# Kernel tuning notes

Hardware: AMD Instinct MI355X
Metric: run time of the kernel (lower is better)

Reference implementation:

```python
import jax, jax.numpy as jnp
import numpy as np

B, C, H, W = 64, 2048, 14, 14
D, S, ITERS, EPS, HID = 256, 8, 3, 1e-8, 512


def build_pos(h, w, d):
    gy, gx = np.meshgrid(np.arange(h), np.arange(w), indexing='ij')
    q = d // 4
    omega = 1.0 / (10000.0 ** (np.arange(q) / q))
    ey = gy.reshape(-1, 1) * omega
    ex = gx.reshape(-1, 1) * omega
    pe = np.concatenate([np.sin(ey), np.cos(ey), np.sin(ex), np.cos(ex)], axis=1)
    return jnp.asarray(pe[None], jnp.float32)  # (1, h*w, d)


def layernorm(x, g, b, eps=1e-5):
    m = x.mean(-1, keepdims=True)
    v = ((x - m) ** 2).mean(-1, keepdims=True)
    return (x - m) * jax.lax.rsqrt(v + eps) * g + b


def setup_inputs() -> dict:
    key = jax.random.key(0)
    ks = jax.random.split(key, 16)
    w = lambda k, shp, s=0.02: jax.random.normal(k, shp, jnp.float32) * s
    inp = {
        'x': jax.random.normal(ks[0], (B, C, H, W), jnp.float32),
        'slot_noise': jax.random.normal(ks[1], (B, S, D), jnp.float32),
        'conv_w': w(ks[2], (C, D)), 'conv_b': jnp.zeros((D,), jnp.float32),
        'pos': build_pos(H, W, D),
        'slots_mu': jax.random.normal(ks[3], (1, 1, D), jnp.float32),
        'slots_logsigma': -jnp.ones((1, 1, D), jnp.float32),
        'qw': w(ks[4], (D, D)), 'qb': jnp.zeros((D,), jnp.float32),
        'kw': w(ks[5], (D, D)), 'kb': jnp.zeros((D,), jnp.float32),
        'vw': w(ks[6], (D, D)), 'vb': jnp.zeros((D,), jnp.float32),
        'gru_wih': w(ks[7], (D, 3 * D)), 'gru_whh': w(ks[8], (D, 3 * D)),
        'gru_bih': jnp.zeros((3 * D,), jnp.float32), 'gru_bhh': jnp.zeros((3 * D,), jnp.float32),
        'w1': w(ks[9], (D, HID)), 'b1': jnp.zeros((HID,), jnp.float32),
        'w2': w(ks[10], (HID, D)), 'b2': jnp.zeros((D,), jnp.float32),
        'ln_in_g': jnp.ones((D,), jnp.float32), 'ln_in_b': jnp.zeros((D,), jnp.float32),
        'ln_s_g': jnp.ones((D,), jnp.float32), 'ln_s_b': jnp.zeros((D,), jnp.float32),
        'ln_ff_g': jnp.ones((D,), jnp.float32), 'ln_ff_b': jnp.zeros((D,), jnp.float32),
    }
    return inp


def reference(x, slot_noise, conv_w, conv_b, pos, slots_mu, slots_logsigma,
              qw, qb, kw, kb, vw, vb, gru_wih, gru_whh, gru_bih, gru_bhh,
              w1, b1, w2, b2, ln_in_g, ln_in_b, ln_s_g, ln_s_b, ln_ff_g, ln_ff_b):
    b, c, h, w_ = x.shape
    d = qw.shape[0]
    scale = d ** (-0.5)
    # (B,C,H,W) -> (B,N,C) -> project -> add pos
    xt = x.transpose(0, 2, 3, 1).reshape(b, h * w_, c)
    xt = xt @ conv_w + conv_b + pos
    # slot init
    slots = slots_mu + jnp.exp(slots_logsigma) * slot_noise  # (B,S,D)
    inp = layernorm(xt, ln_in_g, ln_in_b)
    k = inp @ kw + kb
    v = inp @ vw + vb
    attn = None
    for _ in range(ITERS):
        slots_prev = slots
        s = layernorm(slots, ln_s_g, ln_s_b)
        q = s @ qw + qb
        dots = jnp.einsum('bid,bjd->bij', q, k) * scale  # (B,S,N)
        attn = jax.nn.softmax(dots, axis=1) + EPS  # softmax over slots
        attn = attn / attn.sum(-1, keepdims=True)  # renormalize over keys
        updates = jnp.einsum('bjd,bij->bid', v, attn)  # (B,S,D)
        # GRUCell (torch semantics)
        gi = updates @ gru_wih + gru_bih
        gh = slots_prev @ gru_whh + gru_bhh
        ir, iz, inn = jnp.split(gi, 3, axis=-1)
        hr, hz, hn = jnp.split(gh, 3, axis=-1)
        r = jax.nn.sigmoid(ir + hr)
        z = jax.nn.sigmoid(iz + hz)
        nn_ = jnp.tanh(inn + r * hn)
        slots = (1.0 - z) * nn_ + z * slots_prev
        ff = layernorm(slots, ln_ff_g, ln_ff_b)
        slots = slots + (jax.nn.relu(ff @ w1 + b1)) @ w2 + b2
    attn_map = attn.reshape(b, S, h, w_)
    return slots, attn_map
```

## Files before the change

### kernel.cpp

```cpp
#include <hip/hip_runtime.h>
#include <stdint.h>

#define HWN 196
#define CIN 2048
#define DD  256
#define BB  64
#define NSLOT 8
#define KVPAD 224
#define MTOT 12544
#define BKP 128

typedef __attribute__((ext_vector_type(8))) short short8;
typedef __attribute__((ext_vector_type(4))) float f32x4;
typedef __attribute__((ext_vector_type(4))) unsigned short us4;

__device__ __forceinline__ ushort f2bf(float f){ union{float f;uint32_t u;}v;v.f=f;uint32_t u=v.u;return (ushort)((u+0x7FFFu+((u>>16)&1u))>>16);}
__device__ __forceinline__ float bf2f(ushort h){ union{uint32_t u;float f;}v;v.u=((uint32_t)h)<<16;return v.f;}
__device__ __forceinline__ float sigm(float x){ return 1.f/(1.f+expf(-x)); }

__device__ __forceinline__ short8 ldsY(const ushort* buf, int LD, int kt, int lane){
    int row = lane & 15;
    int ch = kt*4 + (lane>>4);
    return *(const short8*)&buf[row*LD + ((ch ^ (row&7))<<3)];
}
__device__ __forceinline__ short8 gX(const ushort* base, int K, int nrow, int kt, int lane){
    return *(const short8*)&base[(size_t)nrow*K + kt*32 + (lane>>4)*8];
}

struct TD { const float* s; ushort* d; int R, C, t0; };
struct TD8 { TD a[8]; };

__global__ __launch_bounds__(256) void k_prep(TD8 td){
    __shared__ float tile[32][33];
    int bt = blockIdx.x;
    int mi = 0;
    #pragma unroll
    for (int i = 1; i < 8; ++i) if (bt >= td.a[i].t0) mi = i;
    TD d = td.a[mi];
    int lt = bt - d.t0;
    int tilesx = (d.C + 31) >> 5;
    int cb = (lt % tilesx) * 32, rb = (lt / tilesx) * 32;
    int tx = threadIdx.x & 31, ty = threadIdx.x >> 5;
    for (int i = ty; i < 32; i += 8) {
        int r = rb + i, c = cb + tx;
        tile[i][tx] = (r < d.R && c < d.C) ? d.s[(size_t)r * d.C + c] : 0.f;
    }
    __syncthreads();
    for (int i = ty; i < 32; i += 8) {
        int c = cb + i, r = rb + tx;
        if (c < d.C && r < d.R) d.d[(size_t)c * d.R + r] = f2bf(tile[tx][i]);
    }
}

__global__ __launch_bounds__(512) void k_proj(const float* __restrict__ x,
        const ushort* __restrict__ cwT, float* __restrict__ Cpart){
    __shared__ ushort As[2][64*BKP];
    const int t = threadIdx.x, lane = t & 63, wv = t >> 6;
    const int tile = blockIdx.x >> 1, kq = blockIdx.x & 1;
    const int bm = tile * 64;
    const int kbase = kq * 1024;

    const int am = t & 63, kg = t >> 6;
    const int mg = bm + am;
    const int ab = mg / HWN, ap = mg % HWN;
    const float* aptr = x + (size_t)ab*(CIN*HWN) + ap + (size_t)kbase*HWN;

    f32x4 acc[4][2] = {};
    float areg[16];

    #pragma unroll
    for (int j = 0; j < 16; ++j) areg[j] = aptr[(size_t)(kg*16+j)*HWN];
    {
        short8 av0, av1;
        #pragma unroll
        for (int j = 0; j < 8; ++j){ av0[j] = (short)f2bf(areg[j]); av1[j] = (short)f2bf(areg[8+j]); }
        int ch0 = kg*2;
        *(short8*)&As[0][am*BKP + ((ch0^(am&7))<<3)] = av0;
        *(short8*)&As[0][am*BKP + (((ch0+1)^(am&7))<<3)] = av1;
    }
    __syncthreads();
    int cur = 0;
    for (int kt = 0; kt < 8; ++kt){
        if (kt < 7){
            #pragma unroll
            for (int j = 0; j < 16; ++j)
                areg[j] = aptr[(size_t)((kt+1)*BKP + kg*16+j)*HWN];
        }
        short8 bfr[4][2];
        #pragma unroll
        for (int kk = 0; kk < 4; ++kk)
            #pragma unroll
            for (int ni = 0; ni < 2; ++ni){
                int n = wv*32 + ni*16 + (lane&15);
                bfr[kk][ni] = *(const short8*)&cwT[(size_t)n*CIN + kbase + kt*BKP + kk*32 + (lane>>4)*8];
            }
        #pragma unroll
        for (int kk = 0; kk < 4; ++kk){
            short8 afr[4];
            #pragma unroll
            for (int mi = 0; mi < 4; ++mi){
                int row = mi*16 + (lane&15);
                int ch = kk*4 + (lane>>4);
                afr[mi] = *(const short8*)&As[cur][row*BKP + ((ch^(row&7))<<3)];
            }
            #pragma unroll
            for (int mi = 0; mi < 4; ++mi)
                #pragma unroll
                for (int ni = 0; ni < 2; ++ni)
                    acc[mi][ni] = __builtin_amdgcn_mfma_f32_16x16x32_bf16(afr[mi], bfr[kk][ni], acc[mi][ni], 0,0,0);
        }
        if (kt < 7){
            short8 av0, av1;
            #pragma unroll
            for (int j = 0; j < 8; ++j){ av0[j] = (short)f2bf(areg[j]); av1[j] = (short)f2bf(areg[8+j]); }
            int ch0 = kg*2;
            *(short8*)&As[cur^1][am*BKP + ((ch0^(am&7))<<3)] = av0;
            *(short8*)&As[cur^1][am*BKP + (((ch0+1)^(am&7))<<3)] = av1;
        }
        __syncthreads();
        cur ^= 1;
    }
    float* outp = Cpart + (size_t)kq*MTOT*DD;
    #pragma unroll
    for (int mi = 0; mi < 4; ++mi){
        #pragma unroll
        for (int ni = 0; ni < 2; ++ni){
            int n = wv*32 + ni*16 + (lane&15);
            #pragma unroll
            for (int r = 0; r < 4; ++r){
                int m = bm + mi*16 + (lane>>4)*4 + r;
                outp[(size_t)m*DD + n] = acc[mi][ni][r];
            }
        }
    }
}

__global__ __launch_bounds__(512) void k_red(const float* __restrict__ Cpart,
        const float* __restrict__ cb, const float* __restrict__ pos,
        const float* __restrict__ lng, const float* __restrict__ lnb,
        const ushort* __restrict__ kwT, const ushort* __restrict__ vwT,
        const float* __restrict__ kb, const float* __restrict__ vb,
        ushort* __restrict__ kbf, ushort* __restrict__ vT){
    __shared__ ushort As[32*256];
    const int t = threadIdx.x, lane = t & 63, wv = t >> 6;
    const int b = blockIdx.x / 7, pblk = blockIdx.x % 7;
    {
        int row = t >> 4, seg = t & 15;
        int pin = pblk*32 + row;
        int grow = b*HWN + pin;
        if (grow > MTOT-1) grow = MTOT-1;
        int p = pin < HWN ? pin : HWN-1;
        const float* c0 = Cpart + (size_t)grow*DD + seg*16;
        const float* c1 = Cpart + (size_t)MTOT*DD + (size_t)grow*DD + seg*16;
        const float* pp = pos + (size_t)p*DD + seg*16;
        float f[16];
        float s = 0.f, sq = 0.f;
        #pragma unroll
        for (int q = 0; q < 4; ++q){
            f32x4 a  = *(const f32x4*)&c0[q*4];
            f32x4 bq = *(const f32x4*)&c1[q*4];
            f32x4 pv = *(const f32x4*)&pp[q*4];
            f32x4 cv = *(const f32x4*)&cb[seg*16 + q*4];
            #pragma unroll
            for (int r2 = 0; r2 < 4; ++r2){
                float v = a[r2] + bq[r2] + pv[r2] + cv[r2];
                f[q*4+r2] = v; s += v; sq += v*v;
            }
        }
        #pragma unroll
        for (int m = 8; m >= 1; m >>= 1){ s += __shfl_xor(s, m, 64); sq += __shfl_xor(sq, m, 64); }
        float mean = s * (1.f/256.f);
        float rs = rsqrtf(sq*(1.f/256.f) - mean*mean + 1e-5f);
        int d0 = seg*16;
        short8 o0, o1;
        #pragma unroll
        for (int j = 0; j < 8; ++j){
            o0[j] = (short)f2bf((f[j]   - mean)*rs*lng[d0+j]   + lnb[d0+j]);
            o1[j] = (short)f2bf((f[8+j] - mean)*rs*lng[d0+8+j] + lnb[d0+8+j]);
        }
        int ch0 = seg*2;
        *(short8*)&As[row*256 + ((ch0^(row&7))<<3)] = o0;
        *(short8*)&As[row*256 + (((ch0+1)^(row&7))<<3)] = o1;
    }
    __syncthreads();
    f32x4 acck[2][2] = {}, accv[2][2] = {};
    const int n0 = wv*32;
    #pragma unroll
    for (int kt = 0; kt < 8; ++kt){
        short8 afr[2];
        #pragma unroll
        for (int mi = 0; mi < 2; ++mi){
            int row = mi*16 + (lane&15);
            int ch = kt*4 + (lane>>4);
            afr[mi] = *(const short8*)&As[row*256 + ((ch^(row&7))<<3)];
        }
        #pragma unroll
        for (int ni = 0; ni < 2; ++ni){
            int n = n0 + ni*16 + (lane&15);
            int koff = kt*32 + (lane>>4)*8;
            short8 bk = *(const short8*)&kwT[(size_t)n*DD + koff];
            short8 bv = *(const short8*)&vwT[(size_t)n*DD + koff];
            #pragma unroll
            for (int mi = 0; mi < 2; ++mi){
                acck[mi][ni] = __builtin_amdgcn_mfma_f32_16x16x32_bf16(afr[mi], bk, acck[mi][ni],0,0,0);
                accv[mi][ni] = __builtin_amdgcn_mfma_f32_16x16x32_bf16(afr[mi], bv, accv[mi][ni],0,0,0);
            }
        }
    }
    #pragma unroll
    for (int mi = 0; mi < 2; ++mi){
        #pragma unroll
        for (int ni = 0; ni < 2; ++ni){
            int n = n0 + ni*16 + (lane&15);
            float kbn = kb[n], vbn = vb[n];
            int pl0 = pblk*32 + mi*16 + (lane>>4)*4;
            us4 pk;
            #pragma unroll
            for (int r = 0; r < 4; ++r){
                kbf[((size_t)b*KVPAD + pl0 + r)*DD + n] = f2bf(acck[mi][ni][r] + kbn);
                pk[r] = f2bf(accv[mi][ni][r] + vbn);
            }
            *(us4*)&vT[((size_t)b*DD + n)*KVPAD + pl0] = pk;
        }
    }
}

__global__ __launch_bounds__(512) void k_init(const float* __restrict__ noise,
        const float* __restrict__ mu, const float* __restrict__ lsig,
        const ushort* __restrict__ qwT, const float* __restrict__ qb,
        const float* __restrict__ gs, const float* __restrict__ bs,
        float* __restrict__ slots, ushort* __restrict__ qbuf){
    __shared__ float Sld[16*256];
    __shared__ ushort Ysn[16*256];
    __shared__ float part[8][16][2];
    __shared__ float stats[16][2];
    const int t = threadIdx.x, lane = t & 63, w = t >> 6;
    const int bb = blockIdx.x, rbase = bb*16;
    {
        int row = t>>5, ch = t&31; int d = ch*8;
        f32x4 n0 = *(const f32x4*)&noise[(size_t)(rbase+row)*DD + d];
        f32x4 n1 = *(const f32x4*)&noise[(size_t)(rbase+row)*DD + d + 4];
        f32x4 m0 = *(const f32x4*)&mu[d];
        f32x4 m1 = *(const f32x4*)&mu[d+4];
        f32x4 l0 = *(const f32x4*)&lsig[d];
        f32x4 l1 = *(const f32x4*)&lsig[d+4];
        f32x4 s0, s1;
        #pragma unroll
        for (int j = 0; j < 4; ++j){
            s0[j] = m0[j] + expf(l0[j])*n0[j];
            s1[j] = m1[j] + expf(l1[j])*n1[j];
        }
        *(f32x4*)&slots[(size_t)(rbase+row)*DD + d] = s0;
        *(f32x4*)&slots[(size_t)(rbase+row)*DD + d + 4] = s1;
        *(f32x4*)&Sld[row*256 + d] = s0;
        *(f32x4*)&Sld[row*256 + d + 4] = s1;
    }
    __syncthreads();
    f32x4 sv[2];
    #pragma unroll
    for (int sub = 0; sub < 2; ++sub){
        int d0 = w*32 + sub*16 + (lane>>4)*4;
        sv[sub] = *(const f32x4*)&Sld[(lane&15)*256 + d0];
    }
    {
        float lsum = 0.f, lsq = 0.f;
        #pragma unroll
        for (int sub = 0; sub < 2; ++sub)
            #pragma unroll
            for (int r = 0; r < 4; ++r){ float v = sv[sub][r]; lsum += v; lsq += v*v; }
        lsum += __shfl_xor(lsum, 16, 64); lsum += __shfl_xor(lsum, 32, 64);
        lsq  += __shfl_xor(lsq, 16, 64);  lsq  += __shfl_xor(lsq, 32, 64);
        if (lane < 16){ part[w][lane][0] = lsum; part[w][lane][1] = lsq; }
    }
    __syncthreads();
    if (t < 16){
        float a = 0.f, c = 0.f;
        #pragma unroll
        for (int i = 0; i < 8; ++i){ a += part[i][t][0]; c += part[i][t][1]; }
        float mean = a*(1.f/256.f);
        stats[t][0] = mean;
        stats[t][1] = rsqrtf(c*(1.f/256.f) - mean*mean + 1e-5f);
    }
    __syncthreads();
    {
        int slot = lane&15;
        float mean = stats[slot][0], rs = stats[slot][1];
        #pragma unroll
        for (int sub = 0; sub < 2; ++sub){
            int d0 = w*32 + sub*16 + (lane>>4)*4;
            f32x4 g4 = *(const f32x4*)&gs[d0];
            f32x4 b4 = *(const f32x4*)&bs[d0];
            us4 o;
            #pragma unroll
            for (int r = 0; r < 4; ++r) o[r] = f2bf((sv[sub][r]-mean)*rs*g4[r] + b4[r]);
            int ch = d0>>3;
            *(us4*)&Ysn[slot*256 + ((ch^(slot&7))<<3) + (d0&7)] = o;
        }
    }
    __syncthreads();
    f32x4 qa[2] = {};
    #pragma unroll
    for (int kt = 0; kt < 8; ++kt){
        short8 ysn = ldsY(Ysn, 256, kt, lane);
        #pragma unroll
        for (int sub = 0; sub < 2; ++sub){
            int nrow = w*32 + sub*16 + (lane&15);
            short8 xx = gX(qwT, 256, nrow, kt, lane);
            qa[sub] = __builtin_amdgcn_mfma_f32_16x16x32_bf16(xx, ysn, qa[sub], 0,0,0);
        }
    }
    #pragma unroll
    for (int sub = 0; sub < 2; ++sub){
        int qd0 = w*32 + sub*16 + (lane>>4)*4;
        f32x4 qb4 = *(const f32x4*)&qb[qd0];
        us4 o;
        #pragma unroll
        for (int r = 0; r < 4; ++r) o[r] = f2bf((qa[sub][r]+qb4[r])*0.0625f);
        *(us4*)&qbuf[(size_t)(rbase+(lane&15))*DD + qd0] = o;
    }
}

__device__ __forceinline__ float sm_ep(f32x4 acc, int f, int lane, ushort* Xat, int srow){
    int k0 = f*16 + (lane>>4)*4;
    us4 o;
    float ps = 0.f;
    #pragma unroll
    for (int r = 0; r < 4; ++r){
        float v = acc[r];
        float mx = v;
        mx = fmaxf(mx, __shfl_xor(mx, 1, 64));
        mx = fmaxf(mx, __shfl_xor(mx, 2, 64));
        mx = fmaxf(mx, __shfl_xor(mx, 4, 64));
        float e = expf(v - mx);
        float se = e;
        se += __shfl_xor(se, 1, 64);
        se += __shfl_xor(se, 2, 64);
        se += __shfl_xor(se, 4, 64);
        float val = e/se + 1e-8f;
        if (k0 + r >= HWN) val = 0.f;
        ps += val;
        o[r] = f2bf(val);
    }
    int ch = k0 >> 3;
    *(us4*)&Xat[srow*256 + ((ch^(srow&7))<<3) + (k0&7)] = o;
    return ps;
}

__global__ __launch_bounds__(512, 2) void k_slot(
        const ushort* __restrict__ qbuf, const ushort* __restrict__ kbf,
        const ushort* __restrict__ vT, float* __restrict__ slots,
        ushort* __restrict__ qout,
        const ushort* __restrict__ wihT, const ushort* __restrict__ whhT,
        const float* __restrict__ bih, const float* __restrict__ bhh,
        const ushort* __restrict__ w1T, const float* __restrict__ b1,
        const ushort* __restrict__ w2T, const float* __restrict__ b2,
        const float* __restrict__ gff, const float* __restrict__ bff,
        const float* __restrict__ gs, const float* __restrict__ bs,
        const ushort* __restrict__ qwT, const float* __restrict__ qb,
        float* __restrict__ out_slots, float* __restrict__ out_attn,
        int final_){
    __shared__ ushort Yq[16*256];
    __shared__ ushort Xat[16*256];
    __shared__ ushort Yupd[16*256];
    __shared__ ushort Yslb[16*256];
    __shared__ ushort Ysn[16*256];
    __shared__ ushort Yh[16*512];
    __shared__ float wpart[8][16];
    __shared__ float invk[16];
    __shared__ float part[8][16][2];
    __shared__ float stats[16][2];
    const int t = threadIdx.x, lane = t & 63, w = t >> 6;
    const int b = blockIdx.x;
    const int rbase = b * NSLOT;
    const int srow = lane & 15;
    const int srd = (srow < NSLOT) ? srow : 0;

    if (t < 256){
        int row = t>>5, ch = t&31;
        short8 v = *(const short8*)&qbuf[(size_t)(rbase+row)*DD + ch*8];
        *(short8*)&Yq[row*256 + ((ch^(row&7))<<3)] = v;
        f32x4 s0 = *(const f32x4*)&slots[(size_t)(rbase+row)*DD + ch*8];
        f32x4 s1 = *(const f32x4*)&slots[(size_t)(rbase+row)*DD + ch*8 + 4];
        short8 sv;
        #pragma unroll
        for (int j = 0; j < 4; ++j){ sv[j] = (short)f2bf(s0[j]); sv[4+j] = (short)f2bf(s1[j]); }
        *(short8*)&Yslb[row*256 + ((ch^(row&7))<<3)] = sv;
    } else {
        int i = t - 256;
        int row = (i>>5) + 8, ch = i&31;
        short8 z;
        #pragma unroll
        for (int j = 0; j < 8; ++j) z[j] = 0;
        *(short8*)&Yq[row*256 + ((ch^(row&7))<<3)] = z;
        *(short8*)&Yupd[row*256 + ((ch^(row&7))<<3)] = z;
        *(short8*)&Yslb[row*256 + ((ch^(row&7))<<3)] = z;
    }
    __syncthreads();
    {
        short8 yf[8];
        #pragma unroll
        for (int kt = 0; kt < 8; ++kt) yf[kt] = ldsY(Yq, 256, kt, lane);
        const ushort* kb_ = kbf + (size_t)b*KVPAD*DD;
        const int f0 = w, f1 = w + 8;
        const bool v1 = (f1 < 14);
        const int r0 = f0*16 + (lane&15), r1 = f1*16 + (lane&15);
        short8 xa[2], xb[2];
        xa[0] = gX(kb_, 256, r0, 0, lane);
        if (v1) xb[0] = gX(kb_, 256, r1, 0, lane);
        f32x4 accA = {}, accB = {};
        #pragma unroll
        for (int kt = 0; kt < 8; ++kt){
            int cu = kt & 1, nx = cu ^ 1;
            if (kt < 7){
                xa[nx] = gX(kb_, 256, r0, kt+1, lane);
                if (v1) xb[nx] = gX(kb_, 256, r1, kt+1, lane);
            }
            accA = __builtin_amdgcn_mfma_f32_16x16x32_bf16(xa[cu], yf[kt], accA, 0,0,0);
            if (v1) accB = __builtin_amdgcn_mfma_f32_16x16x32_bf16(xb[cu], yf[kt], accB, 0,0,0);
        }
        float ps = sm_ep(accA, f0, lane, Xat, srow);
        if (v1) ps += sm_ep(accB, f1, lane, Xat, srow);
        ps += __shfl_xor(ps, 16, 64);
        ps += __shfl_xor(ps, 32, 64);
        if (lane < 16) wpart[w][lane] = ps;
    }
    __syncthreads();
    if (t < 16){
        float s = 0.f;
        #pragma unroll
        for (int i = 0; i < 8; ++i) s += wpart[i][t];
        invk[t] = 1.f/s;
    }
    f32x4 pvacc[2];
    {
        short8 xat[7];
        #pragma unroll
        for (int kt = 0; kt < 7; ++kt) xat[kt] = ldsY(Xat, 256, kt, lane);
        const ushort* vb_ = vT + (size_t)b*DD*KVPAD;
        const int d0a = (w*2)*16 + (lane&15), d0b = (w*2+1)*16 + (lane&15);
        short8 ya[2], yb[2];
        ya[0] = gX(vb_, KVPAD, d0a, 0, lane);
        yb[0] = gX(vb_, KVPAD, d0b, 0, lane);
        f32x4 aA = {}, aB = {};
        #pragma unroll
        for (int kt = 0; kt < 7; ++kt){
            int cu = kt & 1, nx = cu ^ 1;
            if (kt < 6){
                ya[nx] = gX(vb_, KVPAD, d0a, kt+1, lane);
                yb[nx] = gX(vb_, KVPAD, d0b, kt+1, lane);
            }
            aA = __builtin_amdgcn_mfma_f32_16x16x32_bf16(xat[kt], ya[cu], aA, 0,0,0);
            aB = __builtin_amdgcn_mfma_f32_16x16x32_bf16(xat[kt], yb[cu], aB, 0,0,0);
        }
        pvacc[0] = aA; pvacc[1] = aB;
    }
    __syncthreads();
    {
        f32x4 iv = *(const f32x4*)&invk[(lane>>4)*4];
        #pragma unroll
        for (int i = 0; i < 2; ++i){
            int d0 = (w*2 + i)*16;
            #pragma unroll
            for (int r = 0; r < 4; ++r){
                int s2 = (lane>>4)*4 + r;
                if (s2 < NSLOT){
                    int d = d0 + (lane&15);
                    int ch = d >> 3;
                    Yupd[s2*256 + ((ch^(s2&7))<<3) + (d&7)] = f2bf(pvacc[i][r]*iv[r]);
                }
            }
        }
    }
    if (final_){
        for (int idx = t; idx < NSLOT*HWN; idx += 512){
            int slot = idx/HWN, key = idx - slot*HWN;
            int ch = key >> 3;
            out_attn[(size_t)b*NSLOT*HWN + idx] =
                bf2f(Xat[slot*256 + ((ch^(slot&7))<<3) + (key&7)]) * invk[slot];
        }
    }
    __syncthreads();
    f32x4 gi[6] = {}, gh[6] = {};
    {
        int nrw[6];
        #pragma unroll
        for (int g = 0; g < 3; ++g)
            #pragma unroll
            for (int sub = 0; sub < 2; ++sub)
                nrw[g*2+sub] = g*256 + w*32 + sub*16 + (lane&15);
        short8 xw[2][12];
        #pragma unroll
        for (int j = 0; j < 6; ++j){
            xw[0][j]   = gX(wihT, 256, nrw[j], 0, lane);
            xw[0][6+j] = gX(whhT, 256, nrw[j], 0, lane);
        }
        #pragma unroll
        for (int kt = 0; kt < 8; ++kt){
            int cu = kt & 1, nx = cu ^ 1;
            if (kt < 7){
                #pragma unroll
                for (int j = 0; j < 6; ++j){
                    xw[nx][j]   = gX(wihT, 256, nrw[j], kt+1, lane);
                    xw[nx][6+j] = gX(whhT, 256, nrw[j], kt+1, lane);
                }
            }
            short8 yu = ldsY(Yupd, 256, kt, lane);
            short8 ys = ldsY(Yslb, 256, kt, lane);
            #pragma unroll
            for (int j = 0; j < 6; ++j){
                gi[j] = __builtin_amdgcn_mfma_f32_16x16x32_bf16(xw[cu][j],   yu, gi[j], 0,0,0);
                gh[j] = __builtin_amdgcn_mfma_f32_16x16x32_bf16(xw[cu][6+j], ys, gh[j], 0,0,0);
            }
        }
    }
    f32x4 snew[2];
    #pragma unroll
    for (int sub = 0; sub < 2; ++sub){
        int d0 = w*32 + sub*16 + (lane>>4)*4;
        f32x4 sp  = *(const f32x4*)&slots[(size_t)(rbase + srd)*DD + d0];
        f32x4 bir = *(const f32x4*)&bih[d0];
        f32x4 biz = *(const f32x4*)&bih[256 + d0];
        f32x4 bin = *(const f32x4*)&bih[512 + d0];
        f32x4 bhr = *(const f32x4*)&bhh[d0];
        f32x4 bhz = *(const f32x4*)&bhh[256 + d0];
        f32x4 bhn = *(const f32x4*)&bhh[512 + d0];
        #pragma unroll
        for (int r = 0; r < 4; ++r){
            float ir = gi[0+sub][r] + bir[r];
            float iz = gi[2+sub][r] + biz[r];
            float in_ = gi[4+sub][r] + bin[r];
            float hr = gh[0+sub][r] + bhr[r];
            float hz = gh[2+sub][r] + bhz[r];
            float hn = gh[4+sub][r] + bhn[r];
            float rr = sigm(ir + hr);
            float zz = sigm(iz + hz);
            float nn = tanhf(in_ + rr*hn);
            snew[sub][r] = (1.f - zz)*nn + zz*sp[r];
        }
    }
    {
        float lsum = 0.f, lsq = 0.f;
        #pragma unroll
        for (int sub = 0; sub < 2; ++sub)
            #pragma unroll
            for (int r = 0; r < 4; ++r){ float v = snew[sub][r]; lsum += v; lsq += v*v; }
        lsum += __shfl_xor(lsum, 16, 64); lsum += __shfl_xor(lsum, 32, 64);
        lsq  += __shfl_xor(lsq, 16, 64);  lsq  += __shfl_xor(lsq, 32, 64);
        if (lane < 16){ part[w][lane][0] = lsum; part[w][lane][1] = lsq; }
    }
    __syncthreads();
    if (t < 16){
        float a = 0.f, c = 0.f;
        #pragma unroll
        for (int i = 0; i < 8; ++i){ a += part[i][t][0]; c += part[i][t][1]; }
        float mean = a*(1.f/256.f);
        stats[t][0] = mean;
        stats[t][1] = rsqrtf(c*(1.f/256.f) - mean*mean + 1e-5f);
    }
    __syncthreads();
    {
        float mean = stats[srow][0], rs = stats[srow][1];
        #pragma unroll
        for (int sub = 0; sub < 2; ++sub){
            int d0 = w*32 + sub*16 + (lane>>4)*4;
            f32x4 g4 = *(const f32x4*)&gff[d0];
            f32x4 b4 = *(const f32x4*)&bff[d0];
            us4 o;
            #pragma unroll
            for (int r = 0; r < 4; ++r) o[r] = f2bf((snew[sub][r]-mean)*rs*g4[r] + b4[r]);
            int ch = d0 >> 3;
            *(us4*)&Ysn[srow*256 + ((ch^(srow&7))<<3) + (d0&7)] = o;
        }
    }
    __syncthreads();
    {
        int nr1[4];
        #pragma unroll
        for (int s2 = 0; s2 < 4; ++s2) nr1[s2] = w*64 + s2*16 + (lane&15);
        short8 xw1[2][4];
        #pragma unroll
        for (int s2 = 0; s2 < 4; ++s2) xw1[0][s2] = gX(w1T, 256, nr1[s2], 0, lane);
        f32x4 hh[4] = {};
        #pragma unroll
        for (int kt = 0; kt < 8; ++kt){
            int cu = kt & 1, nx = cu ^ 1;
            if (kt < 7){
                #pragma unroll
                for (int s2 = 0; s2 < 4; ++s2) xw1[nx][s2] = gX(w1T, 256, nr1[s2], kt+1, lane);
            }
            short8 ysn = ldsY(Ysn, 256, kt, lane);
            #pragma unroll
            for (int s2 = 0; s2 < 4; ++s2)
                hh[s2] = __builtin_amdgcn_mfma_f32_16x16x32_bf16(xw1[cu][s2], ysn, hh[s2], 0,0,0);
        }
        #pragma unroll
        for (int s2 = 0; s2 < 4; ++s2){
            int n0 = w*64 + s2*16 + (lane>>4)*4;
            f32x4 b14 = *(const f32x4*)&b1[n0];
            us4 o;
            #pragma unroll
            for (int r = 0; r < 4; ++r) o[r] = f2bf(fmaxf(hh[s2][r] + b14[r], 0.f));
            int ch = n0 >> 3;
            *(us4*)&Yh[srow*512 + ((ch^(srow&7))<<3) + (n0&7)] = o;
        }
    }
    __syncthreads();
    f32x4 ns[2];
    {
        int nr2[2];
        #pragma unroll
        for (int sub = 0; sub < 2; ++sub) nr2[sub] = w*32 + sub*16 + (lane&15);
        short8 xw2[2][2];
        #pragma unroll
        for (int sub = 0; sub < 2; ++sub) xw2[0][sub] = gX(w2T, 512, nr2[sub], 0, lane);
        f32x4 o2[2] = {};
        #pragma unroll
        for (int kt = 0; kt < 16; ++kt){
            int cu = kt & 1, nx = cu ^ 1;
            if (kt < 15){
                #pragma unroll
                for (int sub = 0; sub < 2; ++sub) xw2[nx][sub] = gX(w2T, 512, nr2[sub], kt+1, lane);
            }
            short8 yh = ldsY(Yh, 512, kt, lane);
            #pragma unroll
            for (int sub = 0; sub < 2; ++sub)
                o2[sub] = __builtin_amdgcn_mfma_f32_16x16x32_bf16(xw2[cu][sub], yh, o2[sub], 0,0,0);
        }
        float* dst = final_ ? out_slots : slots;
        #pragma unroll
        for (int sub = 0; sub < 2; ++sub){
            int d0 = w*32 + sub*16 + (lane>>4)*4;
            f32x4 b24 = *(const f32x4*)&b2[d0];
            #pragma unroll
            for (int r = 0; r < 4; ++r) ns[sub][r] = o2[sub][r] + b24[r] + snew[sub][r];
            if (srow < NSLOT)
                *(f32x4*)&dst[(size_t)(rbase + srow)*DD + d0] = ns[sub];
        }
    }
    if (final_) return;
    {
        float lsum = 0.f, lsq = 0.f;
        #pragma unroll
        for (int sub = 0; sub < 2; ++sub)
            #pragma unroll
            for (int r = 0; r < 4; ++r){ float v = ns[sub][r]; lsum += v; lsq += v*v; }
        lsum += __shfl_xor(lsum, 16, 64); lsum += __shfl_xor(lsum, 32, 64);
        lsq  += __shfl_xor(lsq, 16, 64);  lsq  += __shfl_xor(lsq, 32, 64);
        if (lane < 16){ part[w][lane][0] = lsum; part[w][lane][1] = lsq; }
    }
    __syncthreads();
    if (t < 16){
        float a = 0.f, c = 0.f;
        #pragma unroll
        for (int i = 0; i < 8; ++i){ a += part[i][t][0]; c += part[i][t][1]; }
        float mean = a*(1.f/256.f);
        stats[t][0] = mean;
        stats[t][1] = rsqrtf(c*(1.f/256.f) - mean*mean + 1e-5f);
    }
    __syncthreads();
    {
        float mean = stats[srow][0], rs = stats[srow][1];
        #pragma unroll
        for (int sub = 0; sub < 2; ++sub){
            int d0 = w*32 + sub*16 + (lane>>4)*4;
            f32x4 g4 = *(const f32x4*)&gs[d0];
            f32x4 b4 = *(const f32x4*)&bs[d0];
            us4 o;
            #pragma unroll
            for (int r = 0; r < 4; ++r) o[r] = f2bf((ns[sub][r]-mean)*rs*g4[r] + b4[r]);
            int ch = d0 >> 3;
            *(us4*)&Ysn[srow*256 + ((ch^(srow&7))<<3) + (d0&7)] = o;
        }
    }
    __syncthreads();
    {
        int nrq[2];
        #pragma unroll
        for (int sub = 0; sub < 2; ++sub) nrq[sub] = w*32 + sub*16 + (lane&15);
        short8 xq[2][2];
        #pragma unroll
        for (int sub = 0; sub < 2; ++sub) xq[0][sub] = gX(qwT, 256, nrq[sub], 0, lane);
        f32x4 qa[2] = {};
        #pragma unroll
        for (int kt = 0; kt < 8; ++kt){
            int cu = kt & 1, nx = cu ^ 1;
            if (kt < 7){
                #pragma unroll
                for (int sub = 0; sub < 2; ++sub) xq[nx][sub] = gX(qwT, 256, nrq[sub], kt+1, lane);
            }
            short8 ysn = ldsY(Ysn, 256, kt, lane);
            #pragma unroll
            for (int sub = 0; sub < 2; ++sub)
                qa[sub] = __builtin_amdgcn_mfma_f32_16x16x32_bf16(xq[cu][sub], ysn, qa[sub], 0,0,0);
        }
        #pragma unroll
        for (int sub = 0; sub < 2; ++sub){
            int qd0 = w*32 + sub*16 + (lane>>4)*4;
            f32x4 qb4 = *(const f32x4*)&qb[qd0];
            us4 o;
            #pragma unroll
            for (int r = 0; r < 4; ++r) o[r] = f2bf((qa[sub][r]+qb4[r])*0.0625f);
            if (srow < NSLOT)
                *(us4*)&qout[(size_t)(rbase + srow)*DD + qd0] = o;
        }
    }
}

extern "C" void kernel_launch(void* const* d_in, const int* in_sizes, int n_in,
                              void* d_out, int out_size, void* d_ws, size_t ws_size,
                              hipStream_t stream) {
    const float* x      = (const float*)d_in[0];
    const float* noise  = (const float*)d_in[1];
    const float* conv_w = (const float*)d_in[2];
    const float* conv_b = (const float*)d_in[3];
    const float* pos    = (const float*)d_in[4];
    const float* mu     = (const float*)d_in[5];
    const float* logsig = (const float*)d_in[6];
    const float* qw  = (const float*)d_in[7];
    const float* qb  = (const float*)d_in[8];
    const float* kw  = (const float*)d_in[9];
    const float* kb  = (const float*)d_in[10];
    const float* vw  = (const float*)d_in[11];
    const float* vb  = (const float*)d_in[12];
    const float* wih = (const float*)d_in[13];
    const float* whh = (const float*)d_in[14];
    const float* bih = (const float*)d_in[15];
    const float* bhh = (const float*)d_in[16];
    const float* w1  = (const float*)d_in[17];
    const float* b1  = (const float*)d_in[18];
    const float* w2  = (const float*)d_in[19];
    const float* b2  = (const float*)d_in[20];
    const float* g_in = (const float*)d_in[21];
    const float* b_in = (const float*)d_in[22];
    const float* g_s  = (const float*)d_in[23];
    const float* b_s  = (const float*)d_in[24];
    const float* g_ff = (const float*)d_in[25];
    const float* b_ff = (const float*)d_in[26];

    char* w = (char*)d_ws;
    ushort* kbf    = (ushort*)w; w += (size_t)BB*KVPAD*DD*2;
    ushort* vT     = (ushort*)w; w += (size_t)BB*DD*KVPAD*2;
    ushort* cwT    = (ushort*)w; w += (size_t)DD*CIN*2;
    ushort* qwT    = (ushort*)w; w += (size_t)DD*DD*2;
    ushort* kwT    = (ushort*)w; w += (size_t)DD*DD*2;
    ushort* vwT    = (ushort*)w; w += (size_t)DD*DD*2;
    ushort* wihT   = (ushort*)w; w += (size_t)768*DD*2;
    ushort* whhT   = (ushort*)w; w += (size_t)768*DD*2;
    ushort* w1T    = (ushort*)w; w += (size_t)512*DD*2;
    ushort* w2T    = (ushort*)w; w += (size_t)DD*512*2;
    ushort* qbb    = (ushort*)w; w += (size_t)BB*NSLOT*DD*2;
    float*  slotsb = (float*)w;  w += (size_t)BB*NSLOT*DD*4;
    float*  Cpart  = (float*)w;  w += (size_t)2*MTOT*DD*4;

    float* out_slots = (float*)d_out;
    float* out_attn  = (float*)d_out + (size_t)BB*NSLOT*DD;

    TD8 td;
    td.a[0] = { conv_w, cwT, 2048, 256,    0 };
    td.a[1] = { qw,     qwT,  256, 256,  512 };
    td.a[2] = { kw,     kwT,  256, 256,  576 };
    td.a[3] = { vw,     vwT,  256, 256,  640 };
    td.a[4] = { wih,    wihT, 256, 768,  704 };
    td.a[5] = { whh,    whhT, 256, 768,  896 };
    td.a[6] = { w1,     w1T,  256, 512, 1088 };
    td.a[7] = { w2,     w2T,  512, 256, 1216 };

    k_prep<<<1344, 256, 0, stream>>>(td);
    k_proj<<<392, 512, 0, stream>>>(x, cwT, Cpart);
    k_red<<<448, 512, 0, stream>>>(Cpart, conv_b, pos, g_in, b_in,
                                   kwT, vwT, kb, vb, kbf, vT);
    k_init<<<32, 512, 0, stream>>>(noise, mu, logsig, qwT, qb, g_s, b_s, slotsb, qbb);
    for (int it = 0; it < 3; ++it){
        k_slot<<<BB, 512, 0, stream>>>(qbb, kbf, vT, slotsb, qbb,
                                       wihT, whhT, bih, bhh, w1T, b1, w2T, b2,
                                       g_ff, b_ff, g_s, b_s, qwT, qb,
                                       out_slots, out_attn, it == 2);
    }
}
```

Baseline: 243.3 us.

## Retile input projection GEMM per batch image with coalesced vector loads

The 1x1-conv projection kernel now gives each block one batch image (all 196 pixels, padded to 208), half of the output channels and half of K. It replaces the strided scalar pixel loads with coalesced float4 loads of contiguous channel rows. Each wave holds 13 accumulator tiles against a single weight fragment and walks K in 64-wide steps through a transposed LDS tile. This cuts the grid from 392 to 256 blocks, which improves global read coalescing but adds padding waste, scattered scalar LDS stores, and higher register pressure.

```diff
diff --git a/kernel.cpp b/kernel.cpp
--- a/kernel.cpp
+++ b/kernel.cpp
@@ -8,7 +8,7 @@
 #define NSLOT 8
 #define KVPAD 224
 #define MTOT 12544
-#define BKP 128
+#define PPB 208
 
 typedef __attribute__((ext_vector_type(8))) short short8;
 typedef __attribute__((ext_vector_type(4))) float f32x4;
@@ -54,83 +54,72 @@
 
 __global__ __launch_bounds__(512) void k_proj(const float* __restrict__ x,
         const ushort* __restrict__ cwT, float* __restrict__ Cpart){
-    __shared__ ushort As[2][64*BKP];
+    __shared__ ushort As[2][PPB*72];
     const int t = threadIdx.x, lane = t & 63, wv = t >> 6;
-    const int tile = blockIdx.x >> 1, kq = blockIdx.x & 1;
-    const int bm = tile * 64;
-    const int kbase = kq * 1024;
-
-    const int am = t & 63, kg = t >> 6;
-    const int mg = bm + am;
-    const int ab = mg / HWN, ap = mg % HWN;
-    const float* aptr = x + (size_t)ab*(CIN*HWN) + ap + (size_t)kbase*HWN;
-
-    f32x4 acc[4][2] = {};
-    float areg[16];
-
-    #pragma unroll
-    for (int j = 0; j < 16; ++j) areg[j] = aptr[(size_t)(kg*16+j)*HWN];
-    {
-        short8 av0, av1;
-        #pragma unroll
-        for (int j = 0; j < 8; ++j){ av0[j] = (short)f2bf(areg[j]); av1[j] = (short)f2bf(areg[8+j]); }
-        int ch0 = kg*2;
-        *(short8*)&As[0][am*BKP + ((ch0^(am&7))<<3)] = av0;
-        *(short8*)&As[0][am*BKP + (((ch0+1)^(am&7))<<3)] = av1;
+    const int bid = blockIdx.x;
+    const int b = bid >> 2, nh = (bid >> 1) & 1, kq = bid & 1;
+    const int gn = nh*128 + wv*16 + (lane&15);
+    const float* xb = x + (size_t)b*(CIN*HWN) + (size_t)(kq*1024)*HWN;
+    const ushort* cw = cwT + (size_t)gn*CIN + kq*1024 + (lane>>4)*8;
+
+    f32x4 acc[13] = {};
+    f32x4 sreg[7];
+
+    {
+        const f32x4* xs = (const f32x4*)xb;
+        #pragma unroll
+        for (int i = 0; i < 7; ++i){ int idx = t + i*512; if (idx < 3136) sreg[i] = xs[idx]; }
+        #pragma unroll
+        for (int i = 0; i < 7; ++i){
+            int idx = t + i*512;
+            if (idx < 3136){
+                int c = idx/49, p = (idx - c*49)*4;
+                #pragma unroll
+                for (int j = 0; j < 4; ++j) As[0][(p+j)*72 + c] = f2bf(sreg[i][j]);
+            }
+        }
     }
     __syncthreads();
     int cur = 0;
-    for (int kt = 0; kt < 8; ++kt){
-        if (kt < 7){
-            #pragma unroll
-            for (int j = 0; j < 16; ++j)
-                areg[j] = aptr[(size_t)((kt+1)*BKP + kg*16+j)*HWN];
-        }
-        short8 bfr[4][2];
-        #pragma unroll
-        for (int kk = 0; kk < 4; ++kk)
-            #pragma unroll
-            for (int ni = 0; ni < 2; ++ni){
-                int n = wv*32 + ni*16 + (lane&15);
-                bfr[kk][ni] = *(const short8*)&cwT[(size_t)n*CIN + kbase + kt*BKP + kk*32 + (lane>>4)*8];
-            }
-        #pragma unroll
-        for (int kk = 0; kk < 4; ++kk){
-            short8 afr[4];
-            #pragma unroll
-            for (int mi = 0; mi < 4; ++mi){
-                int row = mi*16 + (lane&15);
-                int ch = kk*4 + (lane>>4);
-                afr[mi] = *(const short8*)&As[cur][row*BKP + ((ch^(row&7))<<3)];
-            }
-            #pragma unroll
-            for (int mi = 0; mi < 4; ++mi)
-                #pragma unroll
-                for (int ni = 0; ni < 2; ++ni)
-                    acc[mi][ni] = __builtin_amdgcn_mfma_f32_16x16x32_bf16(afr[mi], bfr[kk][ni], acc[mi][ni], 0,0,0);
-        }
-        if (kt < 7){
-            short8 av0, av1;
-            #pragma unroll
-            for (int j = 0; j < 8; ++j){ av0[j] = (short)f2bf(areg[j]); av1[j] = (short)f2bf(areg[8+j]); }
-            int ch0 = kg*2;
-            *(short8*)&As[cur^1][am*BKP + ((ch0^(am&7))<<3)] = av0;
-            *(short8*)&As[cur^1][am*BKP + (((ch0+1)^(am&7))<<3)] = av1;
+    for (int s = 0; s < 16; ++s){
+        if (s < 15){
+            const f32x4* xs = (const f32x4*)(xb + (size_t)(s+1)*64*HWN);
+            #pragma unroll
+            for (int i = 0; i < 7; ++i){ int idx = t + i*512; if (idx < 3136) sreg[i] = xs[idx]; }
+        }
+        #pragma unroll
+        for (int kk = 0; kk < 2; ++kk){
+            short8 bf = *(const short8*)&cw[s*64 + kk*32];
+            short8 afr[13];
+            #pragma unroll
+            for (int mi = 0; mi < 13; ++mi)
+                afr[mi] = *(const short8*)&As[cur][(mi*16 + (lane&15))*72 + (kk*4 + (lane>>4))*8];
+            #pragma unroll
+            for (int mi = 0; mi < 13; ++mi)
+                acc[mi] = __builtin_amdgcn_mfma_f32_16x16x32_bf16(afr[mi], bf, acc[mi], 0,0,0);
+        }
+        if (s < 15){
+            #pragma unroll
+            for (int i = 0; i < 7; ++i){
+                int idx = t + i*512;
+                if (idx < 3136){
+                    int c = idx/49, p = (idx - c*49)*4;
+                    #pragma unroll
+                    for (int j = 0; j < 4; ++j) As[cur^1][(p+j)*72 + c] = f2bf(sreg[i][j]);
+                }
+            }
         }
         __syncthreads();
         cur ^= 1;
     }
     float* outp = Cpart + (size_t)kq*MTOT*DD;
     #pragma unroll
-    for (int mi = 0; mi < 4; ++mi){
-        #pragma unroll
-        for (int ni = 0; ni < 2; ++ni){
-            int n = wv*32 + ni*16 + (lane&15);
-            #pragma unroll
-            for (int r = 0; r < 4; ++r){
-                int m = bm + mi*16 + (lane>>4)*4 + r;
-                outp[(size_t)m*DD + n] = acc[mi][ni][r];
-            }
+    for (int mi = 0; mi < 13; ++mi){
+        #pragma unroll
+        for (int r = 0; r < 4; ++r){
+            int p = mi*16 + (lane>>4)*4 + r;
+            if (p < HWN)
+                outp[(size_t)(b*HWN + p)*DD + gn] = acc[mi][r];
         }
     }
 }
@@ -766,7 +755,7 @@
     td.a[7] = { w2,     w2T,  512, 256, 1216 };
 
     k_prep<<<1344, 256, 0, stream>>>(td);
-    k_proj<<<392, 512, 0, stream>>>(x, cwT, Cpart);
+    k_proj<<<256, 512, 0, stream>>>(x, cwT, Cpart);
     k_red<<<448, 512, 0, stream>>>(Cpart, conv_b, pos, g_in, b_in,
                                    kwT, vwT, kb, vb, kbf, vT);
     k_init<<<32, 512, 0, stream>>>(noise, mu, logsig, qwT, qb, g_s, b_s, slotsb, qbb);
```

New measurement: 266.9 us. +9.7%, slower.
